# Kernel tuning notes

Hardware: AMD Instinct MI355X
Metric: run time of the kernel (lower is better)

## Reference

```python
import jax, jax.numpy as jnp
import numpy as np


def setup_inputs() -> dict:
    key = jax.random.key(0)
    k1, = jax.random.split(key, 1)
    B, L, D = 128, 1024, 768
    hidden_states = jax.random.normal(k1, (B, L, D), dtype=jnp.float32)
    attention_mask = jnp.zeros((B, 1, 1, L), dtype=jnp.float32)
    return {"hidden_states": hidden_states, "attention_mask": attention_mask, "K": 512}


def reference(hidden_states, attention_mask, K):
    B, L, D = hidden_states.shape
    # r tokens to merge, protected class token (ToMe: r = min(r, (t - protected)//2))
    r = max(0, L - K)
    r = min(r, (L - 1) // 2)

    # --- bipartite soft matching (indices computed under no_grad in torch) ---
    metric = hidden_states / jnp.linalg.norm(hidden_states, axis=-1, keepdims=True)
    a = metric[:, ::2, :]   # [B, t1, D] even tokens (src side)
    b = metric[:, 1::2, :]  # [B, t2, D] odd tokens (dst side)
    scores = jnp.einsum('bid,bjd->bij', a, b)  # [B, t1, t2]
    scores = scores.at[:, 0, :].set(-jnp.inf)  # protect class token (row 0 of src)
    node_max = jnp.max(scores, axis=-1)        # [B, t1]
    node_idx = jnp.argmax(scores, axis=-1)     # [B, t1] best dst per src
    order = jnp.argsort(-node_max, axis=-1)    # descending similarity
    src_idx = order[:, :r]                     # [B, r] tokens to merge away
    unm_idx = jnp.sort(order[:, r:], axis=-1)  # [B, t1-r] kept src tokens (sorted: class_token=True)
    dst_idx = jnp.take_along_axis(node_idx, src_idx, axis=-1)  # [B, r]

    # --- merge(x, mode='mean') with include_self=True ---
    src = hidden_states[:, ::2, :]   # [B, t1, D]
    dst = hidden_states[:, 1::2, :]  # [B, t2, D]
    t2 = dst.shape[1]
    unm = jnp.take_along_axis(src, unm_idx[..., None], axis=1)     # [B, t1-r, D]
    src_g = jnp.take_along_axis(src, src_idx[..., None], axis=1)   # [B, r, D]
    bidx = jnp.arange(B)[:, None]
    dst_sum = dst.at[bidx, dst_idx].add(src_g)                     # self + merged srcs
    counts = jnp.ones((B, t2), dtype=hidden_states.dtype).at[bidx, dst_idx].add(1.0)
    dst_mean = dst_sum / counts[..., None]

    preserved_tokens = jnp.concatenate([unm, dst_mean], axis=1)    # [B, t1-r+t2, D]
    final_attention_mask = jnp.zeros((B, 1, 1, preserved_tokens.shape[1]),
                                     dtype=hidden_states.dtype)
    return preserved_tokens, final_attention_mask
```

## Files before the change

### kernel.cpp

```cpp
#include <hip/hip_runtime.h>
#include <hip/hip_bf16.h>

#define B_ 128
#define L_ 1024
#define T_ 512
#define D_ 768
#define CH_ 96
#define DT_ 513
#define TAU_C 1e-3f
#define PBUF_ 1024

#define A_CSTR 1040
#define A_BYTES (CH_ * A_CSTR)
#define B_CSTR 4112
#define B_BUFB (4 * B_CSTR)
#define B_OFF A_BYTES
#define SMEM_BYTES (A_BYTES + 3 * B_BUFB)

typedef __attribute__((ext_vector_type(8))) short bf16x8;
typedef __attribute__((ext_vector_type(4))) float f32x4;

typedef const __attribute__((address_space(1))) unsigned int* gas1_t;
typedef __attribute__((address_space(3))) unsigned int* gas3_t;

__device__ __forceinline__ unsigned short f2bf_rne(float x){
    unsigned u = __float_as_uint(x);
    unsigned r = (u + 0x7FFFu + ((u >> 16) & 1u)) >> 16;
    return (unsigned short)r;
}

__global__ __launch_bounds__(256) void pack_k(const float* __restrict__ hs,
                                              unsigned short* __restrict__ Apk,
                                              unsigned short* __restrict__ Bpk,
                                              double* __restrict__ nsq,
                                              int* __restrict__ paircnt){
    __shared__ __align__(16) unsigned short LhS[CH_ * 16 * 8];
    if (blockIdx.x == 0 && threadIdx.x == 0) *paircnt = 0;
    int b = blockIdx.x >> 6, g = blockIdx.x & 63;
    int wv = threadIdx.x >> 6, lane = threadIdx.x & 63;

    #pragma unroll
    for (int rr = 0; rr < 4; ++rr){
        int jj = wv * 4 + rr;
        long seq = (long)b * L_ + g * 16 + jj;
        const float4* src = (const float4*)(hs + seq * D_);
        float4 f0 = src[lane], f1 = src[lane + 64], f2 = src[lane + 128];
        double s = 0.0;
        s += (double)f0.x*f0.x + (double)f0.y*f0.y + (double)f0.z*f0.z + (double)f0.w*f0.w;
        s += (double)f1.x*f1.x + (double)f1.y*f1.y + (double)f1.z*f1.z + (double)f1.w*f1.w;
        s += (double)f2.x*f2.x + (double)f2.y*f2.y + (double)f2.z*f2.z + (double)f2.w*f2.w;
        #pragma unroll
        for (int off = 32; off; off >>= 1) s += __shfl_xor(s, off);
        if (lane == 0 && (jj & 1)) nsq[seq] = s;
        float rn = (float)(1.0 / sqrt(s));
        float4 fv[3] = {f0, f1, f2};
        #pragma unroll
        for (int t = 0; t < 3; ++t){
            int e0 = t * 256 + lane * 4;
            int c = e0 >> 3, ei = e0 & 7;
            float vv[4] = {fv[t].x, fv[t].y, fv[t].z, fv[t].w};
            short4 hv;
            #pragma unroll
            for (int e = 0; e < 4; ++e)
                ((short*)&hv)[e] = (short)f2bf_rne(vv[e] * rn);
            int o = c * 128 + ((jj ^ (c & 7)) << 3) + ei;
            *(short4*)(LhS + o) = hv;
        }
    }
    __syncthreads();
    #pragma unroll
    for (int it = 0; it < 6; ++it){
        int linear = it * 256 + threadIdx.x;
        int c = linear >> 4, jj = linear & 15;
        int o = c * 128 + ((jj ^ (c & 7)) << 3);
        int tok = g * 8 + (jj >> 1);
        long go = ((long)(b * CH_ + c) * T_ + tok) * 8;
        if (jj & 1) *(bf16x8*)(Bpk + go) = *(const bf16x8*)(LhS + o);
        else        *(bf16x8*)(Apk + go) = *(const bf16x8*)(LhS + o);
    }
}

__global__ __launch_bounds__(512, 2) void coarse_k(const unsigned short* __restrict__ Apk,
                                                   const unsigned short* __restrict__ Bpk,
                                                   int* __restrict__ node_idx,
                                                   unsigned long long* __restrict__ rowkey,
                                                   int* __restrict__ paircnt,
                                                   int2* __restrict__ pairs){
    __shared__ __align__(16) char SMEM[SMEM_BYTES];

    int bid = blockIdx.x;
    int xcd = bid & 7, q = bid >> 3;
    int it = q & 7, bhi = q >> 3;
    int b = xcd + 8 * bhi;

    int tid = threadIdx.x;
    int w = tid >> 6, lane = tid & 63, l15 = lane & 15, l4 = lane >> 4;

    long pkbase = (long)b * CH_ * T_;

    #pragma unroll
    for (int n = 0; n < 12; ++n){
        int c = w * 12 + n;
        const unsigned short* src = Apk + (pkbase + (long)c * T_ + it * 64 + lane) * 8;
        __builtin_amdgcn_global_load_lds((gas1_t)src, (gas3_t)(SMEM + c * A_CSTR), 16, 0, 0);
    }
    {
        int qq = w, c_rel = qq >> 2, tblk = qq & 3;
        #pragma unroll
        for (int n = 0; n < 2; ++n){
            int q2 = w + 8 * n, cr = q2 >> 2, tb = q2 & 3;
            const unsigned short* s0 = Bpk + (pkbase + (long)cr * T_ + 0 * 256 + tb * 64 + lane) * 8;
            __builtin_amdgcn_global_load_lds((gas1_t)s0, (gas3_t)(SMEM + B_OFF + 0 * B_BUFB + cr * B_CSTR + tb * 1024), 16, 0, 0);
            const unsigned short* s1 = Bpk + (pkbase + (long)cr * T_ + 1 * 256 + tb * 64 + lane) * 8;
            __builtin_amdgcn_global_load_lds((gas1_t)s1, (gas3_t)(SMEM + B_OFF + 1 * B_BUFB + cr * B_CSTR + tb * 1024), 16, 0, 0);
        }
        (void)qq; (void)c_rel; (void)tblk;
    }
    __syncthreads();

    f32x4 acc[4][4];
    #pragma unroll
    for (int i = 0; i < 4; ++i)
        #pragma unroll
        for (int j = 0; j < 4; ++j) acc[i][j] = (f32x4){0.f, 0.f, 0.f, 0.f};

    bf16x8 ah[4];
    #pragma unroll
    for (int ph = 0; ph < 48; ++ph){
        int s = ph >> 1, h = ph & 1, buf = ph % 3;
        if (ph < 46){
            int sn = (ph + 2) >> 1, hn = (ph + 2) & 1, bn = (ph + 2) % 3;
            #pragma unroll
            for (int n = 0; n < 2; ++n){
                int q2 = w + 8 * n, cr = q2 >> 2, tb = q2 & 3;
                const unsigned short* src = Bpk + (pkbase + (long)(sn * 4 + cr) * T_ + hn * 256 + tb * 64 + lane) * 8;
                __builtin_amdgcn_global_load_lds((gas1_t)src, (gas3_t)(SMEM + B_OFF + bn * B_BUFB + cr * B_CSTR + tb * 1024), 16, 0, 0);
            }
        }
        if (h == 0){
            #pragma unroll
            for (int ib = 0; ib < 4; ++ib)
                ah[ib] = *(const bf16x8*)(SMEM + (s * 4 + l4) * A_CSTR + (ib * 16 + l15) * 16);
        }
        bf16x8 bh[2];
        #pragma unroll
        for (int g = 0; g < 2; ++g)
            bh[g] = *(const bf16x8*)(SMEM + B_OFF + buf * B_BUFB + l4 * B_CSTR + (w * 32 + g * 16 + l15) * 16);

        __builtin_amdgcn_s_setprio(1);
        #pragma unroll
        for (int g = 0; g < 2; ++g)
            #pragma unroll
            for (int ib = 0; ib < 4; ++ib)
                acc[ib][h * 2 + g] = __builtin_amdgcn_mfma_f32_16x16x32_bf16(ah[ib], bh[g], acc[ib][h * 2 + g], 0, 0, 0);
        __builtin_amdgcn_s_setprio(0);

        if (ph < 46) asm volatile("s_waitcnt vmcnt(2)" ::: "memory");
        else         asm volatile("s_waitcnt vmcnt(0)" ::: "memory");
        __builtin_amdgcn_s_barrier();
        asm volatile("" ::: "memory");
    }

    float* pm1s = (float*)SMEM;
    int*   pjs  = (int*)(SMEM + 2048);
    float* m1f  = (float*)(SMEM + 4096);
    int*   cnd  = (int*)(SMEM + 4352);
    int2*  pbuf = (int2*)(SMEM + 4608);
    int*   pcnt_s  = (int*)(SMEM + 12800);
    int*   pbase_s = (int*)(SMEM + 12804);

    #pragma unroll
    for (int ib = 0; ib < 4; ++ib)
        #pragma unroll
        for (int rr = 0; rr < 4; ++rr){
            float m1 = -1e30f; int j1 = 0;
            #pragma unroll
            for (int jb2 = 0; jb2 < 4; ++jb2){
                int jb = ((jb2 & 1) << 1) | (jb2 >> 1);
                float v = acc[ib][jb][rr];
                int col = (jb >> 1) * 256 + w * 32 + (jb & 1) * 16 + l15;
                if (v > m1){ m1 = v; j1 = col; }
            }
            #pragma unroll
            for (int m = 1; m < 16; m <<= 1){
                float o1 = __shfl_xor(m1, m);
                int   oj = __shfl_xor(j1, m);
                if (o1 > m1 || (o1 == m1 && oj < j1)){ m1 = o1; j1 = oj; }
            }
            if (l15 == 0){
                int row = ib * 16 + l4 * 4 + rr;
                pm1s[row * 8 + w] = m1; pjs[row * 8 + w] = j1;
            }
        }
    __syncthreads();
    int grow0 = b * T_ + it * 64;
    if (tid < 64){
        float M1 = -1e30f; int J1 = 0;
        #pragma unroll
        for (int w2 = 0; w2 < 8; ++w2){
            float a1 = pm1s[tid * 8 + w2]; int aj = pjs[tid * 8 + w2];
            if (a1 > M1 || (a1 == M1 && aj < J1)){ M1 = a1; J1 = aj; }
        }
        node_idx[grow0 + tid] = J1;
        m1f[tid] = M1;
        cnd[tid] = 0;
        rowkey[grow0 + tid] = 0ULL;
        if (tid == 0) *pcnt_s = 0;
    }
    __syncthreads();
    #pragma unroll
    for (int ib = 0; ib < 4; ++ib)
        #pragma unroll
        for (int rr = 0; rr < 4; ++rr){
            int row = ib * 16 + l4 * 4 + rr;
            float thr_ = m1f[row] - TAU_C;
            int hits = 0;
            #pragma unroll
            for (int jb = 0; jb < 4; ++jb) hits += (acc[ib][jb][rr] > thr_) ? 1 : 0;
            if (hits) atomicAdd(&cnd[row], hits);
        }
    __syncthreads();
    #pragma unroll
    for (int ib = 0; ib < 4; ++ib)
        #pragma unroll
        for (int rr = 0; rr < 4; ++rr){
            int row = ib * 16 + l4 * 4 + rr;
            if (cnd[row] < 2) continue;
            if (it == 0 && row == 0) continue;
            float thr_ = m1f[row] - TAU_C;
            #pragma unroll
            for (int jb = 0; jb < 4; ++jb)
                if (acc[ib][jb][rr] > thr_){
                    int idx = atomicAdd(pcnt_s, 1);
                    int2 pr = make_int2(grow0 + row, (jb >> 1) * 256 + w * 32 + (jb & 1) * 16 + l15);
                    if (idx < PBUF_) pbuf[idx] = pr;
                    else { int p = atomicAdd(paircnt, 1); pairs[p] = pr; }
                }
        }
    __syncthreads();
    if (tid == 0) *pbase_s = atomicAdd(paircnt, min(*pcnt_s, PBUF_));
    __syncthreads();
    int n = min(*pcnt_s, PBUF_);
    for (int k2 = tid; k2 < n; k2 += 512) pairs[*pbase_s + k2] = pbuf[k2];
}

__global__ __launch_bounds__(256) void refine_k(const float* __restrict__ hs,
                                                const double* __restrict__ nsq,
                                                const int* __restrict__ paircnt,
                                                const int2* __restrict__ pairs,
                                                unsigned long long* __restrict__ rowkey){
    int n = *paircnt;
    int w = threadIdx.x >> 6, lane = threadIdx.x & 63;
    for (int p = blockIdx.x * 4 + w; p < n; p += gridDim.x * 4){
        int2 pr = pairs[p];
        int grow = pr.x, j = pr.y;
        int b = grow >> 9, i = grow & 511;
        const float* ar = hs + ((long)b * L_ + 2 * i) * D_;
        const float* br = hs + ((long)b * L_ + 2 * j + 1) * D_;
        double s = 0.0;
        #pragma unroll
        for (int dd = 0; dd < 12; ++dd){
            int d = dd * 64 + lane;
            s += (double)ar[d] * (double)br[d];
        }
        #pragma unroll
        for (int off = 32; off; off >>= 1) s += __shfl_xor(s, off);
        if (lane == 0){
            double sc = s / sqrt(nsq[(long)b * L_ + 2 * j + 1]);
            unsigned long long bits = (unsigned long long)__double_as_longlong(sc);
            unsigned long long key = (bits >> 63) ? ~bits : (bits | 0x8000000000000000ULL);
            key = (key & ~0xFFFFULL) | (unsigned long long)(511 - j);
            atomicMax(&rowkey[grow], key);
        }
    }
}

__global__ __launch_bounds__(512) void csr_k(const int* __restrict__ node_idx,
                                             const unsigned long long* __restrict__ rowkey,
                                             int* __restrict__ goff,
                                             int* __restrict__ glist){
    __shared__ int sidx[512];
    __shared__ int off[513];
    __shared__ int tmp[512];
    __shared__ int cnt[512];
    int b = blockIdx.x, t = threadIdx.x;
    unsigned long long rk = rowkey[b * T_ + t];
    sidx[t] = rk ? (511 - (int)(rk & 0xFFFFULL)) : node_idx[b * T_ + t];
    cnt[t] = 0;
    __syncthreads();
    if (t >= 1) atomicAdd(&cnt[sidx[t]], 1);
    __syncthreads();
    tmp[t] = cnt[t];
    __syncthreads();
    for (int s = 1; s < 512; s <<= 1){
        int v = (t >= s) ? tmp[t - s] : 0;
        __syncthreads();
        tmp[t] += v;
        __syncthreads();
    }
    if (t == 0) off[0] = 0;
    off[t + 1] = tmp[t];
    __syncthreads();
    if (t >= 1){
        int j = sidx[t], r = 0;
        for (int i2 = 1; i2 < t; ++i2) r += (sidx[i2] == j);
        glist[b * T_ + off[j] + r] = t;
    }
    goff[b * 513 + t] = off[t];
    if (t == 0) goff[b * 513 + 512] = off[512];
}

__global__ __launch_bounds__(192) void merge_k(const float* __restrict__ hs,
                                               const int* __restrict__ goff,
                                               const int* __restrict__ glist,
                                               float* __restrict__ out){
    int bid = blockIdx.x;
    int b = bid / DT_, jj = bid - b * DT_;
    long obase4 = ((long)b * DT_ + jj) * (D_ / 4);
    float4* out4 = (float4*)out;
    if (threadIdx.x == 0) out[(long)B_ * DT_ * D_ + b * DT_ + jj] = 0.0f;
    int d = threadIdx.x;
    if (jj == 0){
        const float4* src = (const float4*)(hs + (long)b * L_ * D_);
        out4[obase4 + d] = src[d];
        return;
    }
    int j = jj - 1;
    int o0 = goff[b * 513 + j], o1 = goff[b * 513 + j + 1];
    const float4* dst = (const float4*)(hs + ((long)b * L_ + 2 * j + 1) * D_);
    float4 a = dst[d];
    for (int s = o0; s < o1; ++s){
        int i = glist[b * T_ + s];
        const float4* srow = (const float4*)(hs + ((long)b * L_ + 2 * i) * D_);
        float4 v = srow[d];
        a.x += v.x; a.y += v.y; a.z += v.z; a.w += v.w;
    }
    float rc = 1.0f / (float)(o1 - o0 + 1);
    a.x *= rc; a.y *= rc; a.z *= rc; a.w *= rc;
    out4[obase4 + d] = a;
}

extern "C" void kernel_launch(void* const* d_in, const int* in_sizes, int n_in,
                              void* d_out, int out_size, void* d_ws, size_t ws_size,
                              hipStream_t stream){
    const float* hs = (const float*)d_in[0];
    float* out = (float*)d_out;
    char* ws = (char*)d_ws;

    const long PSZ = (long)B_ * CH_ * T_ * 8;
    unsigned short* Apk = (unsigned short*)ws;
    unsigned short* Bpk = Apk + PSZ;
    double* nsq      = (double*)(ws + 201326592);
    int*    node_idx = (int*)   (ws + 202375168);
    unsigned long long* rowkey = (unsigned long long*)(ws + 202637312);
    int*    paircnt  = (int*)   (ws + 203161600);
    int*    goff     = (int*)   (ws + 203161856);
    int*    glist    = (int*)   (ws + 203425024);
    int2*   pairs    = (int2*)  (ws + 203687168);

    pack_k  <<<B_ * 64, 256, 0, stream>>>(hs, Apk, Bpk, nsq, paircnt);
    coarse_k<<<B_ * 8, 512, 0, stream>>>(Apk, Bpk, node_idx, rowkey, paircnt, pairs);
    refine_k<<<512, 256, 0, stream>>>(hs, nsq, paircnt, pairs, rowkey);
    csr_k   <<<B_, 512, 0, stream>>>(node_idx, rowkey, goff, glist);
    merge_k <<<B_ * DT_, 192, 0, stream>>>(hs, goff, glist, out);
}
```

Before: 369.0 us.

## Stream A and B tiles per k-step through 4-slot LDS ring buffer

Before, the coarse GEMM kernel loaded the whole A tile up front and then streamed B in half-width phases through a 3-slot buffer, with a full barrier before compute began. Now each k-step loads both A and B for the full 512-column width into one slot of a 4-deep ring, prefetching 3 steps ahead. This halves the number of barrier iterations and overlaps the A load with compute, at the cost of more outstanding loads and 4-byte A transfers. It also reduces the per-row hit count with wave shuffles before the LDS atomic.

```diff
diff --git a/kernel.cpp b/kernel.cpp
--- a/kernel.cpp
+++ b/kernel.cpp
@@ -10,12 +10,12 @@
 #define TAU_C 1e-3f
 #define PBUF_ 1024
 
-#define A_CSTR 1040
-#define A_BYTES (CH_ * A_CSTR)
-#define B_CSTR 4112
-#define B_BUFB (4 * B_CSTR)
-#define B_OFF A_BYTES
-#define SMEM_BYTES (A_BYTES + 3 * B_BUFB)
+#define KS_B_CSTR 8208
+#define KS_B_BYTES (4 * KS_B_CSTR)
+#define KS_A_CSTR 1040
+#define KS_A_BYTES (4 * KS_A_CSTR)
+#define KS_BYTES (KS_B_BYTES + KS_A_BYTES)
+#define SMEM_BYTES (4 * KS_BYTES)
 
 typedef __attribute__((ext_vector_type(8))) short bf16x8;
 typedef __attribute__((ext_vector_type(4))) float f32x4;
@@ -97,26 +97,24 @@
     int w = tid >> 6, lane = tid & 63, l15 = lane & 15, l4 = lane >> 4;
 
     long pkbase = (long)b * CH_ * T_;
-
-    #pragma unroll
-    for (int n = 0; n < 12; ++n){
-        int c = w * 12 + n;
-        const unsigned short* src = Apk + (pkbase + (long)c * T_ + it * 64 + lane) * 8;
-        __builtin_amdgcn_global_load_lds((gas1_t)src, (gas3_t)(SMEM + c * A_CSTR), 16, 0, 0);
-    }
-    {
-        int qq = w, c_rel = qq >> 2, tblk = qq & 3;
-        #pragma unroll
-        for (int n = 0; n < 2; ++n){
-            int q2 = w + 8 * n, cr = q2 >> 2, tb = q2 & 3;
-            const unsigned short* s0 = Bpk + (pkbase + (long)cr * T_ + 0 * 256 + tb * 64 + lane) * 8;
-            __builtin_amdgcn_global_load_lds((gas1_t)s0, (gas3_t)(SMEM + B_OFF + 0 * B_BUFB + cr * B_CSTR + tb * 1024), 16, 0, 0);
-            const unsigned short* s1 = Bpk + (pkbase + (long)cr * T_ + 1 * 256 + tb * 64 + lane) * 8;
-            __builtin_amdgcn_global_load_lds((gas1_t)s1, (gas3_t)(SMEM + B_OFF + 1 * B_BUFB + cr * B_CSTR + tb * 1024), 16, 0, 0);
-        }
-        (void)qq; (void)c_rel; (void)tblk;
-    }
-    __syncthreads();
+    int ca = w >> 1, tb4a = (w & 1) << 1;
+
+    #define STAGE(s_, slot_) do {                                                          \
+        char* dst_ = SMEM + (slot_) * KS_BYTES;                                            \
+        _Pragma("unroll")                                                                  \
+        for (int n_ = 0; n_ < 4; ++n_){                                                    \
+            const unsigned short* sp_ = Bpk + (pkbase + (long)((s_)*4 + n_) * T_ + w * 64 + lane) * 8; \
+            __builtin_amdgcn_global_load_lds((gas1_t)sp_, (gas3_t)(dst_ + n_ * KS_B_CSTR + w * 1024), 16, 0, 0); \
+        }                                                                                  \
+        _Pragma("unroll")                                                                  \
+        for (int n_ = 0; n_ < 2; ++n_){                                                    \
+            int tb_ = tb4a + n_;                                                           \
+            const unsigned short* sp_ = Apk + (pkbase + (long)((s_)*4 + ca) * T_ + it * 64 + tb_ * 16) * 8 + lane * 2; \
+            __builtin_amdgcn_global_load_lds((gas1_t)sp_, (gas3_t)(dst_ + KS_B_BYTES + ca * KS_A_CSTR + tb_ * 256), 4, 0, 0); \
+        }                                                                                  \
+    } while (0)
+
+    STAGE(0, 0); STAGE(1, 1); STAGE(2, 2);
 
     f32x4 acc[4][4];
     #pragma unroll
@@ -124,42 +122,33 @@
         #pragma unroll
         for (int j = 0; j < 4; ++j) acc[i][j] = (f32x4){0.f, 0.f, 0.f, 0.f};
 
-    bf16x8 ah[4];
-    #pragma unroll
-    for (int ph = 0; ph < 48; ++ph){
-        int s = ph >> 1, h = ph & 1, buf = ph % 3;
-        if (ph < 46){
-            int sn = (ph + 2) >> 1, hn = (ph + 2) & 1, bn = (ph + 2) % 3;
-            #pragma unroll
-            for (int n = 0; n < 2; ++n){
-                int q2 = w + 8 * n, cr = q2 >> 2, tb = q2 & 3;
-                const unsigned short* src = Bpk + (pkbase + (long)(sn * 4 + cr) * T_ + hn * 256 + tb * 64 + lane) * 8;
-                __builtin_amdgcn_global_load_lds((gas1_t)src, (gas3_t)(SMEM + B_OFF + bn * B_BUFB + cr * B_CSTR + tb * 1024), 16, 0, 0);
-            }
-        }
-        if (h == 0){
+    __syncthreads();
+
+    #pragma unroll 4
+    for (int s = 0; s < 24; ++s){
+        if (s < 21) STAGE(s + 3, (s + 3) & 3);
+        const char* slot = SMEM + (s & 3) * KS_BYTES;
+        bf16x8 ah[4], bh[4];
+        #pragma unroll
+        for (int ib = 0; ib < 4; ++ib)
+            ah[ib] = *(const bf16x8*)(slot + KS_B_BYTES + l4 * KS_A_CSTR + (ib * 16 + l15) * 16);
+        #pragma unroll
+        for (int jb = 0; jb < 4; ++jb)
+            bh[jb] = *(const bf16x8*)(slot + l4 * KS_B_CSTR + (w * 64 + jb * 16 + l15) * 16);
+        __builtin_amdgcn_s_setprio(1);
+        #pragma unroll
+        for (int jb = 0; jb < 4; ++jb)
             #pragma unroll
             for (int ib = 0; ib < 4; ++ib)
-                ah[ib] = *(const bf16x8*)(SMEM + (s * 4 + l4) * A_CSTR + (ib * 16 + l15) * 16);
-        }
-        bf16x8 bh[2];
-        #pragma unroll
-        for (int g = 0; g < 2; ++g)
-            bh[g] = *(const bf16x8*)(SMEM + B_OFF + buf * B_BUFB + l4 * B_CSTR + (w * 32 + g * 16 + l15) * 16);
-
-        __builtin_amdgcn_s_setprio(1);
-        #pragma unroll
-        for (int g = 0; g < 2; ++g)
-            #pragma unroll
-            for (int ib = 0; ib < 4; ++ib)
-                acc[ib][h * 2 + g] = __builtin_amdgcn_mfma_f32_16x16x32_bf16(ah[ib], bh[g], acc[ib][h * 2 + g], 0, 0, 0);
+                acc[ib][jb] = __builtin_amdgcn_mfma_f32_16x16x32_bf16(ah[ib], bh[jb], acc[ib][jb], 0, 0, 0);
         __builtin_amdgcn_s_setprio(0);
-
-        if (ph < 46) asm volatile("s_waitcnt vmcnt(2)" ::: "memory");
-        else         asm volatile("s_waitcnt vmcnt(0)" ::: "memory");
+        if (s <= 20)      asm volatile("s_waitcnt vmcnt(12)" ::: "memory");
+        else if (s == 21) asm volatile("s_waitcnt vmcnt(6)"  ::: "memory");
+        else              asm volatile("s_waitcnt vmcnt(0)"  ::: "memory");
         __builtin_amdgcn_s_barrier();
         asm volatile("" ::: "memory");
     }
+    #undef STAGE
 
     float* pm1s = (float*)SMEM;
     int*   pjs  = (int*)(SMEM + 2048);
@@ -175,10 +164,9 @@
         for (int rr = 0; rr < 4; ++rr){
             float m1 = -1e30f; int j1 = 0;
             #pragma unroll
-            for (int jb2 = 0; jb2 < 4; ++jb2){
-                int jb = ((jb2 & 1) << 1) | (jb2 >> 1);
+            for (int jb = 0; jb < 4; ++jb){
                 float v = acc[ib][jb][rr];
-                int col = (jb >> 1) * 256 + w * 32 + (jb & 1) * 16 + l15;
+                int col = w * 64 + jb * 16 + l15;
                 if (v > m1){ m1 = v; j1 = col; }
             }
             #pragma unroll
@@ -217,7 +205,9 @@
             int hits = 0;
             #pragma unroll
             for (int jb = 0; jb < 4; ++jb) hits += (acc[ib][jb][rr] > thr_) ? 1 : 0;
-            if (hits) atomicAdd(&cnd[row], hits);
+            #pragma unroll
+            for (int m = 1; m < 16; m <<= 1) hits += __shfl_xor(hits, m);
+            if (l15 == 0 && hits) atomicAdd(&cnd[row], hits);
         }
     __syncthreads();
     #pragma unroll
@@ -232,7 +222,7 @@
             for (int jb = 0; jb < 4; ++jb)
                 if (acc[ib][jb][rr] > thr_){
                     int idx = atomicAdd(pcnt_s, 1);
-                    int2 pr = make_int2(grow0 + row, (jb >> 1) * 256 + w * 32 + (jb & 1) * 16 + l15);
+                    int2 pr = make_int2(grow0 + row, w * 64 + jb * 16 + l15);
                     if (idx < PBUF_) pbuf[idx] = pr;
                     else { int p = atomicAdd(paircnt, 1); pairs[p] = pr; }
                 }
```

Measured after the change: 365.7 us. About the same (-0.9%).
